# Performance work log

Hardware: AMD Instinct MI355X
Metric: run time of the kernel (lower is better)

The kernel has to match this reference:

```python
import jax, jax.numpy as jnp
import numpy as np
from jax import lax

SEQ, F, H1, H2, B, WV, OBJ, REL, VOCAB = 33, 20480, 900, 900, 2, 100, 35, 82, 117


def setup_inputs() -> dict:
    key = jax.random.key(0)
    ks = jax.random.split(key, 17)
    s = lambda k, shape: jax.random.normal(k, shape, jnp.float32) * 0.02
    return dict(
        x=jax.random.normal(ks[0], (SEQ, B, F), jnp.float32),
        w_ih1=s(ks[1], (4 * H1, F)), w_hh1=s(ks[2], (4 * H1, H1)),
        b_ih1=s(ks[3], (4 * H1,)), b_hh1=s(ks[4], (4 * H1,)),
        w_ih2=s(ks[5], (SEQ, 4 * H2, H1 + WV)), w_hh2=s(ks[6], (SEQ, 4 * H2, H2)),
        b_ih2=s(ks[7], (SEQ, 4 * H2)), b_hh2=s(ks[8], (SEQ, 4 * H2)),
        w_obj1=s(ks[9], (OBJ, H2)), b_obj1=s(ks[10], (OBJ,)),
        w_rel=s(ks[11], (REL, H2)), b_rel=s(ks[12], (REL,)),
        w_obj2=s(ks[13], (OBJ, H2)), b_obj2=s(ks[14], (OBJ,)),
        embed=s(ks[15], (VOCAB, WV)),
    )


def lstm_cell(xt, h, c, w_ih, w_hh, b_ih, b_hh):
    # torch gate order: input, forget, cell(g), output
    gates = xt @ w_ih.T + h @ w_hh.T + b_ih + b_hh
    i, f, g, o = jnp.split(gates, 4, axis=-1)
    c = jax.nn.sigmoid(f) * c + jax.nn.sigmoid(i) * jnp.tanh(g)
    h = jax.nn.sigmoid(o) * jnp.tanh(c)
    return h, c


def reference(x, w_ih1, w_hh1, b_ih1, b_hh1, w_ih2, w_hh2, b_ih2, b_hh2,
              w_obj1, b_obj1, w_rel, b_rel, w_obj2, b_obj2, embed):
    batch = x.shape[1]
    # layer-1 LSTM over full sequence
    def step1(carry, xt):
        h, c = lstm_cell(xt, carry[0], carry[1], w_ih1, w_hh1, b_ih1, b_hh1)
        return (h, c), h
    h0 = jnp.zeros((batch, H1), x.dtype)
    _, out1 = lax.scan(step1, (h0, h0), x)  # [SEQ, B, H1]

    # layer-2: first SEQ-2 cells with zero word vector, distinct weights per step
    wv0 = jnp.zeros((batch, WV), x.dtype)
    def step2(carry, inp):
        xt, wih, whh, bih, bhh = inp
        h, c = lstm_cell(jnp.concatenate([xt, wv0], axis=1), carry[0], carry[1], wih, whh, bih, bhh)
        return (h, c), None
    h20 = jnp.zeros((batch, H2), x.dtype)
    (h2, c2), _ = lax.scan(step2, (h20, h20),
                           (out1[:SEQ - 2], w_ih2[:SEQ - 2], w_hh2[:SEQ - 2],
                            b_ih2[:SEQ - 2], b_hh2[:SEQ - 2]))

    obj1 = h2 @ w_obj1.T + b_obj1                      # [B, 35]
    wv = embed[jnp.argmax(obj1, axis=1)]               # [B, 100]
    h2, c2 = lstm_cell(jnp.concatenate([out1[SEQ - 2], wv], axis=1), h2, c2,
                       w_ih2[SEQ - 2], w_hh2[SEQ - 2], b_ih2[SEQ - 2], b_hh2[SEQ - 2])

    rel = h2 @ w_rel.T + b_rel                         # [B, 82]
    wv = embed[jnp.argmax(rel, axis=1) + OBJ]
    h2, c2 = lstm_cell(jnp.concatenate([out1[SEQ - 1], wv], axis=1), h2, c2,
                       w_ih2[SEQ - 1], w_hh2[SEQ - 1], b_ih2[SEQ - 1], b_hh2[SEQ - 1])

    obj2 = h2 @ w_obj2.T + b_obj2                      # [B, 35]
    return (obj1, rel, obj2)
```

## Files before the change

kernel.cpp:

```cpp
#include <hip/hip_runtime.h>

#define SEQn 33
#define Fn   20480
#define Hn   900
#define Bn   2
#define WVn  100
#define OBJn 35
#define RELn 82
#define G4n  3600
#define Mn   66
#define NBLK 225
#define NITV 37

#define KS1  16
#define KSL1 (Fn/KS1)
#define RB1  15
#define RPB1 240
#define NC1  (KSL1/32)
#define WSTR 40

typedef __attribute__((ext_vector_type(8))) short bf16x8;
typedef __attribute__((ext_vector_type(4))) float f32x4;

__device__ __forceinline__ float sigf(float v){ return 1.f/(1.f+expf(-v)); }
__device__ __forceinline__ float dot4(float4 a, float4 b){ return a.x*b.x+a.y*b.y+a.z*b.z+a.w*b.w; }
__device__ __forceinline__ float wred(float v){
  #pragma unroll
  for (int d = 32; d >= 1; d >>= 1) v += __shfl_xor(v, d, 64);
  return v;
}
__device__ __forceinline__ float gload(const float* p){
  return __hip_atomic_load((const float*)p, __ATOMIC_RELAXED, __HIP_MEMORY_SCOPE_AGENT);
}
__device__ __forceinline__ void gstore(float* p, float v){
  __hip_atomic_store(p, v, __ATOMIC_RELAXED, __HIP_MEMORY_SCOPE_AGENT);
}
__device__ __forceinline__ unsigned short f2bf(float f){
  unsigned u = __float_as_uint(f);
  unsigned r = u + 0x7FFFu + ((u >> 16) & 1u);
  return (unsigned short)(r >> 16);
}
__device__ __forceinline__ float bf2f(unsigned short h){
  return __uint_as_float(((unsigned)h) << 16);
}

__device__ __forceinline__ void gbar(unsigned* bar){
  __syncthreads();
  if (threadIdx.x == 0) {
    unsigned g = __hip_atomic_load(&bar[0], __ATOMIC_RELAXED, __HIP_MEMORY_SCOPE_AGENT);
    unsigned cnt = __hip_atomic_fetch_add(&bar[32], 1u, __ATOMIC_RELAXED, __HIP_MEMORY_SCOPE_AGENT);
    if (cnt == (unsigned)(NBLK-1)) {
      __hip_atomic_store(&bar[32], 0u, __ATOMIC_RELAXED, __HIP_MEMORY_SCOPE_AGENT);
      asm volatile("s_waitcnt vmcnt(0)" ::: "memory");
      __hip_atomic_store(&bar[0], g+1u, __ATOMIC_RELAXED, __HIP_MEMORY_SCOPE_AGENT);
    } else {
      unsigned cur;
      do {
        __builtin_amdgcn_s_sleep(8);
        cur = __hip_atomic_load(&bar[0], __ATOMIC_RELAXED, __HIP_MEMORY_SCOPE_AGENT);
      } while (cur == g);
    }
  }
  __syncthreads();
}

__global__ __launch_bounds__(320) void k1_mfma(
    const float* __restrict__ x, const float* __restrict__ w1,
    float* __restrict__ G1, unsigned* __restrict__ bar)
{
  const int tid = threadIdx.x;
  if (blockIdx.x == 0 && tid == 0) {
    __hip_atomic_store(&bar[0], 0u, __ATOMIC_RELAXED, __HIP_MEMORY_SCOPE_AGENT);
    __hip_atomic_store(&bar[32], 0u, __ATOMIC_RELAXED, __HIP_MEMORY_SCOPE_AGENT);
  }
  __shared__ unsigned short WhL[2][RPB1*WSTR], WlL[2][RPB1*WSTR];
  __shared__ unsigned short XhL[2][80*WSTR],  XlL[2][80*WSTR];

  const int rb = blockIdx.x % RB1;
  const int ks = blockIdx.x / RB1;
  const int r0 = rb * RPB1;
  const int kofs = ks * KSL1;
  const int wv_ = tid >> 6;
  const int lane = tid & 63;
  const int p = lane & 15;
  const int q = lane >> 4;

  f32x4 acc[3][5];
  #pragma unroll
  for (int rt = 0; rt < 3; ++rt)
    #pragma unroll
    for (int mt = 0; mt < 5; ++mt) acc[rt][mt] = (f32x4){0.f,0.f,0.f,0.f};

  float4 wr[6], xrg[2];

  #define ISSUE_STAGE(cc)                                                      \
    { const int kbase = kofs + (cc)*32;                                        \
      _Pragma("unroll")                                                        \
      for (int u = 0; u < 6; ++u) {                                            \
        const int idx = tid + u*320;                                           \
        const int row = idx >> 3, k4 = idx & 7;                                \
        wr[u] = *(const float4*)(w1 + (size_t)(r0+row)*Fn + kbase + k4*4);     \
      }                                                                        \
      _Pragma("unroll")                                                        \
      for (int u = 0; u < 2; ++u) {                                            \
        const int idx = tid + u*320;                                           \
        const int mrow = idx >> 3, k4 = idx & 7;                               \
        xrg[u] = (mrow < Mn)                                                   \
          ? *(const float4*)(x + (size_t)mrow*Fn + kbase + k4*4)               \
          : make_float4(0.f,0.f,0.f,0.f);                                      \
      }                                                                        \
    }

  #define CVTW(dsth, dstl, off, v)                                             \
    { const unsigned short h0=f2bf(v.x), h1=f2bf(v.y), h2=f2bf(v.z), h3=f2bf(v.w); \
      const unsigned short l0=f2bf(v.x-bf2f(h0)), l1=f2bf(v.y-bf2f(h1));       \
      const unsigned short l2=f2bf(v.z-bf2f(h2)), l3=f2bf(v.w-bf2f(h3));       \
      *(uint2*)&dsth[off] = make_uint2((unsigned)h0|((unsigned)h1<<16),        \
                                       (unsigned)h2|((unsigned)h3<<16));       \
      *(uint2*)&dstl[off] = make_uint2((unsigned)l0|((unsigned)l1<<16),        \
                                       (unsigned)l2|((unsigned)l3<<16));       \
    }

  #define WRITE_STAGE(bb)                                                     \
    { _Pragma("unroll")                                                       \
      for (int u = 0; u < 6; ++u) {                                           \
        const int idx = tid + u*320;                                          \
        const int row = idx >> 3, k4 = idx & 7;                               \
        CVTW(WhL[bb], WlL[bb], row*WSTR + k4*4, wr[u]);                       \
      }                                                                       \
      _Pragma("unroll")                                                       \
      for (int u = 0; u < 2; ++u) {                                           \
        const int idx = tid + u*320;                                          \
        const int mrow = idx >> 3, k4 = idx & 7;                              \
        CVTW(XhL[bb], XlL[bb], mrow*WSTR + k4*4, xrg[u]);                     \
      }                                                                       \
    }

  ISSUE_STAGE(0);
  WRITE_STAGE(0);
  __syncthreads();

  for (int c = 0; c < NC1; ++c) {
    const int buf = c & 1;
    if (c+1 < NC1) ISSUE_STAGE(c+1);

    bf16x8 Bh[5], Bl[5];
    #pragma unroll
    for (int mt = 0; mt < 5; ++mt) {
      const int moff = (mt*16 + p)*WSTR + q*8;
      Bh[mt] = *(const bf16x8*)&XhL[buf][moff];
      Bl[mt] = *(const bf16x8*)&XlL[buf][moff];
    }
    #pragma unroll
    for (int rt = 0; rt < 3; ++rt) {
      const int roff = ((wv_ + 5*rt)*16 + p)*WSTR + q*8;
      const bf16x8 Ah = *(const bf16x8*)&WhL[buf][roff];
      const bf16x8 Al = *(const bf16x8*)&WlL[buf][roff];
      #pragma unroll
      for (int mt = 0; mt < 5; ++mt) {
        acc[rt][mt] = __builtin_amdgcn_mfma_f32_16x16x32_bf16(Ah, Bh[mt], acc[rt][mt], 0, 0, 0);
        acc[rt][mt] = __builtin_amdgcn_mfma_f32_16x16x32_bf16(Ah, Bl[mt], acc[rt][mt], 0, 0, 0);
        acc[rt][mt] = __builtin_amdgcn_mfma_f32_16x16x32_bf16(Al, Bh[mt], acc[rt][mt], 0, 0, 0);
      }
    }

    if (c+1 < NC1) WRITE_STAGE(buf^1);
    __syncthreads();
  }

  #pragma unroll
  for (int rt = 0; rt < 3; ++rt)
    #pragma unroll
    for (int mt = 0; mt < 5; ++mt) {
      const int m = mt*16 + p;
      if (m < Mn) {
        #pragma unroll
        for (int r4 = 0; r4 < 4; ++r4) {
          const int grow = r0 + (wv_ + 5*rt)*16 + q*4 + r4;
          atomicAdd(&G1[(size_t)grow*Mn + m], acc[rt][mt][r4]);
        }
      }
    }
  #undef ISSUE_STAGE
  #undef WRITE_STAGE
  #undef CVTW
}

__global__ __launch_bounds__(512) void k_rec(
    const float* __restrict__ G1, float* __restrict__ out1, float* __restrict__ h2buf,
    const float* __restrict__ whh1,
    const float* __restrict__ wih2, const float* __restrict__ whh2,
    const float* __restrict__ bih2, const float* __restrict__ bhh2,
    const float* __restrict__ bih1, const float* __restrict__ bhh1,
    const float* __restrict__ wobj1, const float* __restrict__ bobj1,
    const float* __restrict__ wrel,  const float* __restrict__ brel,
    const float* __restrict__ wobj2, const float* __restrict__ bobj2,
    const float* __restrict__ embed, float* __restrict__ dout,
    unsigned* __restrict__ bar)
{
  __shared__ float hls[Bn][904];
  __shared__ float h2l[Bn][904];
  __shared__ float wvls[Bn][104];
  __shared__ float gls[16][68];
  __shared__ float bls[SEQn][16];
  __shared__ float gexA[16][Bn], gexB[16][Bn];
  __shared__ float cA[4][Bn], cB[4][Bn];
  __shared__ float red[4];
  __shared__ int idxls[Bn];

  const int tid = threadIdx.x;
  const int blk = blockIdx.x;
  const int j0 = blk * 4;
  const int wv_ = tid >> 6;
  const int lane = tid & 63;

  if (tid < 8) {
    const int jj = tid >> 1, m = tid & 1;
    cA[jj][m] = 0.f; cB[jj][m] = 0.f;
    gstore(h2buf + (size_t)m*Hn + j0 + jj, 0.f);
  }

  for (int qq = tid; qq < 16*Mn; qq += 512) {
    const int rho = qq / Mn, t = qq % Mn;
    const int gate = rho >> 2, jj = rho & 3;
    const size_t rA = (size_t)gate*Hn + j0 + jj;
    gls[rho][t] = G1[rA*Mn + t] + bih1[rA] + bhh1[rA];
  }
  for (int qq = tid; qq < SEQn*16; qq += 512) {
    const int s = qq / 16, rho = qq % 16;
    const int gate = rho >> 2, jj = rho & 3;
    const size_t ro = (size_t)s*G4n + (size_t)gate*Hn + j0 + jj;
    bls[s][rho] = bih2[ro] + bhh2[ro];
  }

  float4 wAreg[2][4];
  #pragma unroll
  for (int ri = 0; ri < 2; ++ri) {
    const int rho = wv_*2 + ri;
    const int gate = rho >> 2, jj = rho & 3;
    const size_t row = (size_t)gate*Hn + j0 + jj;
    #pragma unroll
    for (int e = 0; e < 4; ++e) {
      const int k = lane*4 + e*256;
      wAreg[ri][e] = (k <= Hn-4) ? *(const float4*)(whh1 + row*Hn + k)
                                 : make_float4(0.f,0.f,0.f,0.f);
    }
  }

  float4 wiR[2][4], whR[2][4];
  #define ISSUE_W(sp)                                                        \
    { _Pragma("unroll")                                                      \
      for (int ri = 0; ri < 2; ++ri) {                                       \
        const int rho = wv_*2 + ri;                                          \
        const int gate = rho >> 2, jj = rho & 3;                             \
        const size_t ro = (size_t)(sp)*G4n + (size_t)gate*Hn + j0 + jj;      \
        const float* wI = wih2 + ro*1000;                                    \
        const float* wH = whh2 + ro*Hn;                                      \
        _Pragma("unroll")                                                    \
        for (int e = 0; e < 4; ++e) {                                        \
          const int k = lane*4 + e*256;                                      \
          if (k <= 996) wiR[ri][e] = *(const float4*)(wI + k);               \
          if (k <= 896) whR[ri][e] = *(const float4*)(wH + k);               \
        }                                                                    \
      }                                                                      \
    }
  ISSUE_W(0);

  for (int i = 0; i < NITV; ++i) {
    const bool hasA = (i <= 32);
    const int  s = (i >= 1 && i <= 31) ? (i-1) : (i == 33) ? 31 : (i == 35) ? 32 : -1;
    const bool hasB = (s >= 0);

    if (i == 33 || i == 35) {
      if (wv_ < 2) {
        const int m = wv_;
        const int nout = (i == 33) ? OBJn : RELn;
        const int off = (i == 33) ? 0 : Bn*OBJn;
        float v = -1e30f; int idx = 0;
        for (int o = lane; o < nout; o += 64) {
          float t = gload(dout + off + m*nout + o);
          if (t > v) { v = t; idx = o; }
        }
        #pragma unroll
        for (int d = 32; d >= 1; d >>= 1) {
          float ov = __shfl_xor(v, d, 64);
          int   oi = __shfl_xor(idx, d, 64);
          if (ov > v || (ov == v && oi < idx)) { v = ov; idx = oi; }
        }
        if (lane == 0) idxls[m] = idx + ((i == 35) ? OBJn : 0);
      }
      __syncthreads();
      for (int qq = tid; qq < Bn*104; qq += 512) {
        const int m = qq / 104, v4 = qq % 104;
        wvls[m][v4] = (v4 < WVn) ? embed[(size_t)idxls[m]*WVn + v4] : 0.f;
      }
      __syncthreads();
    }

    const bool stageH = hasA || (i == 35);
    const int  srcA = (i == 35) ? 32 : i-1;
    if (stageH) {
      for (int qq = tid; qq < 1808; qq += 512) {
        const int m = qq / 904, kk = qq % 904;
        hls[m][kk] = (i > 0 && kk < 900)
          ? gload(out1 + ((size_t)srcA*Bn + m)*Hn + kk) : 0.f;
      }
    }
    if (hasB) {
      for (int qq = tid; qq < 1808; qq += 512) {
        const int m = qq / 904, kk = qq % 904;
        h2l[m][kk] = (kk < 900)
          ? gload(h2buf + ((size_t)(s&1)*Bn + m)*Hn + kk) : 0.f;
      }
    }
    __syncthreads();

    if (hasA) {
      #pragma unroll
      for (int ri = 0; ri < 2; ++ri) {
        const int rho = wv_*2 + ri;
        float a0 = 0.f, a1 = 0.f;
        #pragma unroll
        for (int e = 0; e < 4; ++e) {
          const int k = lane*4 + e*256;
          if (k <= Hn-4) {
            a0 += dot4(wAreg[ri][e], *(const float4*)&hls[0][k]);
            a1 += dot4(wAreg[ri][e], *(const float4*)&hls[1][k]);
          }
        }
        a0 = wred(a0); a1 = wred(a1);
        if (lane == 0) {
          gexA[rho][0] = a0 + gls[rho][i*Bn + 0];
          gexA[rho][1] = a1 + gls[rho][i*Bn + 1];
        }
      }
    }

    if (hasB) {
      #pragma unroll
      for (int ri = 0; ri < 2; ++ri) {
        const int rho = wv_*2 + ri;
        float b0 = 0.f, b1 = 0.f;
        #pragma unroll
        for (int e = 0; e < 4; ++e) {
          const int k = lane*4 + e*256;
          if (k <= 896) {
            b0 += dot4(wiR[ri][e], *(const float4*)&hls[0][k]);
            b1 += dot4(wiR[ri][e], *(const float4*)&hls[1][k]);
            b0 += dot4(whR[ri][e], *(const float4*)&h2l[0][k]);
            b1 += dot4(whR[ri][e], *(const float4*)&h2l[1][k]);
          } else if (k >= 900 && k <= 996 && s >= SEQn-2) {
            b0 += dot4(wiR[ri][e], *(const float4*)&wvls[0][k-900]);
            b1 += dot4(wiR[ri][e], *(const float4*)&wvls[1][k-900]);
          }
        }
        b0 = wred(b0); b1 = wred(b1);
        if (lane == 0) {
          const float bb = bls[s][rho];
          gexB[rho][0] = b0 + bb;
          gexB[rho][1] = b1 + bb;
        }
      }
      if (s < 32) ISSUE_W(s+1);
    }

    if (i == 32 || i == 34 || i == 36) {
      const int nout = (i == 34) ? RELn : OBJn;
      const float* wh  = (i == 32) ? wobj1 : (i == 34) ? wrel : wobj2;
      const float* bh_ = (i == 32) ? bobj1 : (i == 34) ? brel : bobj2;
      const int off = (i == 32) ? 0 : (i == 34) ? (Bn*OBJn) : (Bn*OBJn + Bn*RELn);
      const int hb = (i == 34) ? 0 : 1;
      if (blk < nout*Bn) {
        const int o = blk >> 1, m = blk & 1;
        float p = 0.f;
        if (tid < 225) {
          const float4 wv4 = *(const float4*)(wh + (size_t)o*Hn + tid*4);
          float* hp = h2buf + ((size_t)hb*Bn + m)*Hn + tid*4;
          p = wv4.x*gload(hp+0) + wv4.y*gload(hp+1)
            + wv4.z*gload(hp+2) + wv4.w*gload(hp+3);
        }
        if (wv_ < 4) {
          const float pr = wred(p);
          if (lane == 0) red[wv_] = pr;
        }
        __syncthreads();
        if (tid == 0)
          gstore(&dout[off + m*nout + o], red[0]+red[1]+red[2]+red[3] + bh_[o]);
      }
    }

    __syncthreads();
    if (tid < 8) {
      const int jj = tid >> 1, m = tid & 1;
      if (hasA) {
        const float cc = sigf(gexA[4+jj][m])*cA[jj][m]
                       + sigf(gexA[jj][m])*tanhf(gexA[8+jj][m]);
        cA[jj][m] = cc;
        gstore(out1 + ((size_t)i*Bn + m)*Hn + j0 + jj, sigf(gexA[12+jj][m])*tanhf(cc));
      }
      if (hasB) {
        const float cc = sigf(gexB[4+jj][m])*cB[jj][m]
                       + sigf(gexB[jj][m])*tanhf(gexB[8+jj][m]);
        cB[jj][m] = cc;
        gstore(h2buf + ((size_t)((s+1)&1)*Bn + m)*Hn + j0 + jj,
               sigf(gexB[12+jj][m])*tanhf(cc));
      }
    }

    if (i < NITV-1) gbar(bar);
  }
  #undef ISSUE_W
}

extern "C" void kernel_launch(void* const* d_in, const int* in_sizes, int n_in,
                              void* d_out, int out_size, void* d_ws, size_t ws_size,
                              hipStream_t stream)
{
  (void)in_sizes; (void)n_in; (void)out_size; (void)ws_size;
  const float* x     = (const float*)d_in[0];
  const float* wih1  = (const float*)d_in[1];
  const float* whh1  = (const float*)d_in[2];
  const float* bih1  = (const float*)d_in[3];
  const float* bhh1  = (const float*)d_in[4];
  const float* wih2  = (const float*)d_in[5];
  const float* whh2  = (const float*)d_in[6];
  const float* bih2  = (const float*)d_in[7];
  const float* bhh2  = (const float*)d_in[8];
  const float* wobj1 = (const float*)d_in[9];
  const float* bobj1 = (const float*)d_in[10];
  const float* wrel  = (const float*)d_in[11];
  const float* brel  = (const float*)d_in[12];
  const float* wobj2 = (const float*)d_in[13];
  const float* bobj2 = (const float*)d_in[14];
  const float* embed = (const float*)d_in[15];
  float* dout = (float*)d_out;

  float* ws = (float*)d_ws;
  float* G1    = ws;
  float* out1  = G1 + (size_t)G4n*Mn;
  float* h2buf = out1 + (size_t)SEQn*Bn*Hn;
  unsigned* bar = (unsigned*)(h2buf + (size_t)2*Bn*Hn);

  hipMemsetAsync(G1, 0, (size_t)G4n*Mn*sizeof(float), stream);
  hipLaunchKernelGGL(k1_mfma, dim3(RB1*KS1), dim3(320), 0, stream, x, wih1, G1, bar);

  void* args[19];
  args[0]  = (void*)&G1;    args[1]  = (void*)&out1;  args[2]  = (void*)&h2buf;
  args[3]  = (void*)&whh1;  args[4]  = (void*)&wih2;  args[5]  = (void*)&whh2;
  args[6]  = (void*)&bih2;  args[7]  = (void*)&bhh2;  args[8]  = (void*)&bih1;
  args[9]  = (void*)&bhh1;  args[10] = (void*)&wobj1; args[11] = (void*)&bobj1;
  args[12] = (void*)&wrel;  args[13] = (void*)&brel;  args[14] = (void*)&wobj2;
  args[15] = (void*)&bobj2; args[16] = (void*)&embed; args[17] = (void*)&dout;
  args[18] = (void*)&bar;
  hipLaunchCooperativeKernel((void*)k_rec, dim3(NBLK), dim3(512), args, 0, stream);
}
```

Measured before the change: 564.6 us.

## Double-buffer layer-2 weight prefetch and peel the steady-state recurrent loop

Splits the persistent recurrent loop into a peeled first step, a fully unrolled steady-state section (iterations 1-31) and a tail section for the argmax and head steps. Layer-2 per-step weights are now double-buffered in two register sets, and the next step's loads are issued before the current step's dot products instead of after them. This gives those loads a whole iteration plus a grid barrier to arrive, and the steady section drops the per-iteration branch logic. The cost is twice the weight registers per thread, which risks spilling or lower occupancy.

```diff
diff --git a/kernel.cpp b/kernel.cpp
--- a/kernel.cpp
+++ b/kernel.cpp
@@ -10,7 +10,6 @@
 #define G4n  3600
 #define Mn   66
 #define NBLK 225
-#define NITV 37
 
 #define KS1  16
 #define KSL1 (Fn/KS1)
@@ -55,9 +54,8 @@
       __hip_atomic_store(&bar[0], g+1u, __ATOMIC_RELAXED, __HIP_MEMORY_SCOPE_AGENT);
     } else {
       unsigned cur;
-      do {
-        __builtin_amdgcn_s_sleep(8);
-        cur = __hip_atomic_load(&bar[0], __ATOMIC_RELAXED, __HIP_MEMORY_SCOPE_AGENT);
+      do { __builtin_amdgcn_s_sleep(8);
+           cur = __hip_atomic_load(&bar[0], __ATOMIC_RELAXED, __HIP_MEMORY_SCOPE_AGENT);
       } while (cur == g);
     }
   }
@@ -247,8 +245,8 @@
     }
   }
 
-  float4 wiR[2][4], whR[2][4];
-  #define ISSUE_W(sp)                                                        \
+  float4 wiR0[2][4], whR0[2][4], wiR1[2][4], whR1[2][4];
+  #define ISSUE_W(sp, WI, WH)                                                \
     { _Pragma("unroll")                                                      \
       for (int ri = 0; ri < 2; ++ri) {                                       \
         const int rho = wv_*2 + ri;                                          \
@@ -259,18 +257,122 @@
         _Pragma("unroll")                                                    \
         for (int e = 0; e < 4; ++e) {                                        \
           const int k = lane*4 + e*256;                                      \
-          if (k <= 996) wiR[ri][e] = *(const float4*)(wI + k);               \
-          if (k <= 896) whR[ri][e] = *(const float4*)(wH + k);               \
+          if (k <= 996) WI[ri][e] = *(const float4*)(wI + k);                \
+          if (k <= 896) WH[ri][e] = *(const float4*)(wH + k);                \
         }                                                                    \
       }                                                                      \
     }
-  ISSUE_W(0);
-
-  for (int i = 0; i < NITV; ++i) {
-    const bool hasA = (i <= 32);
-    const int  s = (i >= 1 && i <= 31) ? (i-1) : (i == 33) ? 31 : (i == 35) ? 32 : -1;
-    const bool hasB = (s >= 0);
-
+
+  #define ADOTS(ivar)                                                        \
+    { _Pragma("unroll")                                                      \
+      for (int ri = 0; ri < 2; ++ri) {                                       \
+        const int rho = wv_*2 + ri;                                          \
+        float a0 = 0.f, a1 = 0.f;                                            \
+        _Pragma("unroll")                                                    \
+        for (int e = 0; e < 4; ++e) {                                        \
+          const int k = lane*4 + e*256;                                      \
+          if (k <= Hn-4) {                                                   \
+            a0 += dot4(wAreg[ri][e], *(const float4*)&hls[0][k]);            \
+            a1 += dot4(wAreg[ri][e], *(const float4*)&hls[1][k]);            \
+          }                                                                  \
+        }                                                                    \
+        a0 = wred(a0); a1 = wred(a1);                                        \
+        if (lane == 0) {                                                     \
+          gexA[rho][0] = a0 + gls[rho][(ivar)*Bn + 0];                       \
+          gexA[rho][1] = a1 + gls[rho][(ivar)*Bn + 1];                       \
+        }                                                                    \
+      }                                                                      \
+    }
+
+  #define BDOTS(svar, WI, WH, USEWV)                                         \
+    { _Pragma("unroll")                                                      \
+      for (int ri = 0; ri < 2; ++ri) {                                       \
+        const int rho = wv_*2 + ri;                                          \
+        float b0 = 0.f, b1 = 0.f;                                            \
+        _Pragma("unroll")                                                    \
+        for (int e = 0; e < 4; ++e) {                                        \
+          const int k = lane*4 + e*256;                                      \
+          if (k <= 896) {                                                    \
+            b0 += dot4(WI[ri][e], *(const float4*)&hls[0][k]);               \
+            b1 += dot4(WI[ri][e], *(const float4*)&hls[1][k]);               \
+            b0 += dot4(WH[ri][e], *(const float4*)&h2l[0][k]);               \
+            b1 += dot4(WH[ri][e], *(const float4*)&h2l[1][k]);               \
+          } else if ((USEWV) && k >= 900 && k <= 996) {                      \
+            b0 += dot4(WI[ri][e], *(const float4*)&wvls[0][k-900]);          \
+            b1 += dot4(WI[ri][e], *(const float4*)&wvls[1][k-900]);          \
+          }                                                                  \
+        }                                                                    \
+        b0 = wred(b0); b1 = wred(b1);                                        \
+        if (lane == 0) {                                                     \
+          const float bb = bls[svar][rho];                                   \
+          gexB[rho][0] = b0 + bb;                                            \
+          gexB[rho][1] = b1 + bb;                                            \
+        }                                                                    \
+      }                                                                      \
+    }
+
+  #define UPD_A(ivar)                                                        \
+    { const float cc = sigf(gexA[4+jj][m])*cA[jj][m]                         \
+                     + sigf(gexA[jj][m])*tanhf(gexA[8+jj][m]);               \
+      cA[jj][m] = cc;                                                        \
+      gstore(out1 + ((size_t)(ivar)*Bn + m)*Hn + j0 + jj,                    \
+             sigf(gexA[12+jj][m])*tanhf(cc)); }
+
+  #define UPD_B(svar)                                                        \
+    { const float cc = sigf(gexB[4+jj][m])*cB[jj][m]                         \
+                     + sigf(gexB[jj][m])*tanhf(gexB[8+jj][m]);               \
+      cB[jj][m] = cc;                                                        \
+      gstore(h2buf + ((size_t)(((svar)+1)&1)*Bn + m)*Hn + j0 + jj,           \
+             sigf(gexB[12+jj][m])*tanhf(cc)); }
+
+  #define STAGE_STEADY(ivar)                                                 \
+    { for (int qq = tid; qq < 1808; qq += 512) {                             \
+        const int m = qq / 904, kk = qq % 904;                               \
+        hls[m][kk] = (kk < 900)                                              \
+          ? gload(out1 + ((size_t)((ivar)-1)*Bn + m)*Hn + kk) : 0.f;         \
+      }                                                                      \
+      for (int qq = tid; qq < 1808; qq += 512) {                             \
+        const int m = qq / 904, kk = qq % 904;                               \
+        h2l[m][kk] = (kk < 900)                                              \
+          ? gload(h2buf + ((size_t)(((ivar)-1)&1)*Bn + m)*Hn + kk) : 0.f;    \
+      } }
+
+  #define STEADY(ivar, WIu, WHu, WIa, WHa)                                   \
+    { STAGE_STEADY(ivar);                                                    \
+      __syncthreads();                                                       \
+      ISSUE_W((ivar), WIa, WHa);                                             \
+      ADOTS(ivar);                                                           \
+      BDOTS((ivar)-1, WIu, WHu, 0);                                          \
+      __syncthreads();                                                       \
+      if (tid < 8) {                                                         \
+        const int jj = tid >> 1, m = tid & 1;                                \
+        UPD_A(ivar);                                                         \
+        UPD_B((ivar)-1);                                                     \
+      }                                                                      \
+      gbar(bar); }
+
+  ISSUE_W(0, wiR0, whR0);
+  __syncthreads();
+
+  if (lane == 0) {
+    #pragma unroll
+    for (int ri = 0; ri < 2; ++ri) {
+      const int rho = wv_*2 + ri;
+      gexA[rho][0] = gls[rho][0];
+      gexA[rho][1] = gls[rho][1];
+    }
+  }
+  __syncthreads();
+  if (tid < 8) { const int jj = tid >> 1, m = tid & 1; UPD_A(0); }
+  gbar(bar);
+
+  for (int ib = 1; ib <= 29; ib += 2) {
+    STEADY(ib,   wiR0, whR0, wiR1, whR1);
+    STEADY(ib+1, wiR1, whR1, wiR0, whR0);
+  }
+  STEADY(31, wiR0, whR0, wiR1, whR1);
+
+  for (int i = 32; i < 37; ++i) {
     if (i == 33 || i == 35) {
       if (wv_ < 2) {
         const int m = wv_;
@@ -297,12 +399,15 @@
       __syncthreads();
     }
 
-    const bool stageH = hasA || (i == 35);
+    const bool hasA = (i == 32);
+    const int  s = (i == 33) ? 31 : (i == 35) ? 32 : -1;
+    const bool hasB = (s >= 0);
     const int  srcA = (i == 35) ? 32 : i-1;
-    if (stageH) {
+
+    if (hasA || i == 35) {
       for (int qq = tid; qq < 1808; qq += 512) {
         const int m = qq / 904, kk = qq % 904;
-        hls[m][kk] = (i > 0 && kk < 900)
+        hls[m][kk] = (kk < 900)
           ? gload(out1 + ((size_t)srcA*Bn + m)*Hn + kk) : 0.f;
       }
     }
@@ -315,54 +420,9 @@
     }
     __syncthreads();
 
-    if (hasA) {
-      #pragma unroll
-      for (int ri = 0; ri < 2; ++ri) {
-        const int rho = wv_*2 + ri;
-        float a0 = 0.f, a1 = 0.f;
-        #pragma unroll
-        for (int e = 0; e < 4; ++e) {
-          const int k = lane*4 + e*256;
-          if (k <= Hn-4) {
-            a0 += dot4(wAreg[ri][e], *(const float4*)&hls[0][k]);
-            a1 += dot4(wAreg[ri][e], *(const float4*)&hls[1][k]);
-          }
-        }
-        a0 = wred(a0); a1 = wred(a1);
-        if (lane == 0) {
-          gexA[rho][0] = a0 + gls[rho][i*Bn + 0];
-          gexA[rho][1] = a1 + gls[rho][i*Bn + 1];
-        }
-      }
-    }
-
-    if (hasB) {
-      #pragma unroll
-      for (int ri = 0; ri < 2; ++ri) {
-        const int rho = wv_*2 + ri;
-        float b0 = 0.f, b1 = 0.f;
-        #pragma unroll
-        for (int e = 0; e < 4; ++e) {
-          const int k = lane*4 + e*256;
-          if (k <= 896) {
-            b0 += dot4(wiR[ri][e], *(const float4*)&hls[0][k]);
-            b1 += dot4(wiR[ri][e], *(const float4*)&hls[1][k]);
-            b0 += dot4(whR[ri][e], *(const float4*)&h2l[0][k]);
-            b1 += dot4(whR[ri][e], *(const float4*)&h2l[1][k]);
-          } else if (k >= 900 && k <= 996 && s >= SEQn-2) {
-            b0 += dot4(wiR[ri][e], *(const float4*)&wvls[0][k-900]);
-            b1 += dot4(wiR[ri][e], *(const float4*)&wvls[1][k-900]);
-          }
-        }
-        b0 = wred(b0); b1 = wred(b1);
-        if (lane == 0) {
-          const float bb = bls[s][rho];
-          gexB[rho][0] = b0 + bb;
-          gexB[rho][1] = b1 + bb;
-        }
-      }
-      if (s < 32) ISSUE_W(s+1);
-    }
+    if (hasA) ADOTS(32);
+    if (i == 33) { BDOTS(31, wiR1, whR1, 1); ISSUE_W(32, wiR0, whR0); }
+    if (i == 35) { BDOTS(32, wiR0, whR0, 1); }
 
     if (i == 32 || i == 34 || i == 36) {
       const int nout = (i == 34) ? RELn : OBJn;
@@ -392,24 +452,20 @@
     __syncthreads();
     if (tid < 8) {
       const int jj = tid >> 1, m = tid & 1;
-      if (hasA) {
-        const float cc = sigf(gexA[4+jj][m])*cA[jj][m]
-                       + sigf(gexA[jj][m])*tanhf(gexA[8+jj][m]);
-        cA[jj][m] = cc;
-        gstore(out1 + ((size_t)i*Bn + m)*Hn + j0 + jj, sigf(gexA[12+jj][m])*tanhf(cc));
-      }
-      if (hasB) {
-        const float cc = sigf(gexB[4+jj][m])*cB[jj][m]
-                       + sigf(gexB[jj][m])*tanhf(gexB[8+jj][m]);
-        cB[jj][m] = cc;
-        gstore(h2buf + ((size_t)((s+1)&1)*Bn + m)*Hn + j0 + jj,
-               sigf(gexB[12+jj][m])*tanhf(cc));
-      }
-    }
-
-    if (i < NITV-1) gbar(bar);
+      if (hasA) UPD_A(32);
+      if (i == 33) UPD_B(31);
+      if (i == 35) UPD_B(32);
+    }
+
+    if (i < 36) gbar(bar);
   }
   #undef ISSUE_W
+  #undef ADOTS
+  #undef BDOTS
+  #undef UPD_A
+  #undef UPD_B
+  #undef STAGE_STEADY
+  #undef STEADY
 }
 
 extern "C" void kernel_launch(void* const* d_in, const int* in_sizes, int n_in,
```

Measured after the change: 675.2 us. +19.6%, slower.

## Specialize recurrent steady-state loop with direct global loads and lighter grid barrier

Applied to the files above, without the earlier changes.

Splits the 37-iteration recurrence into a peeled first step, a specialized loop for steps 1–31 and a tail for the head/argmax steps. The steady-state loop reads h vectors straight from global memory into registers instead of staging them in LDS, and replaces the double-buffered h2 with a per-step history array so reads and writes never alias. It also uses a lighter grid barrier built on raw s_barrier and a shorter sleep in the spin loop. The aim is to cut per-step synchronisation and LDS staging latency on the serial critical path, at the cost of relying on relaxed atomics and waitcnt for memory ordering, which is more fragile.

```diff
diff --git a/kernel.cpp b/kernel.cpp
--- a/kernel.cpp
+++ b/kernel.cpp
@@ -10,7 +10,6 @@
 #define G4n  3600
 #define Mn   66
 #define NBLK 225
-#define NITV 37
 
 #define KS1  16
 #define KSL1 (Fn/KS1)
@@ -55,13 +54,38 @@
       __hip_atomic_store(&bar[0], g+1u, __ATOMIC_RELAXED, __HIP_MEMORY_SCOPE_AGENT);
     } else {
       unsigned cur;
-      do {
-        __builtin_amdgcn_s_sleep(8);
-        cur = __hip_atomic_load(&bar[0], __ATOMIC_RELAXED, __HIP_MEMORY_SCOPE_AGENT);
+      do { __builtin_amdgcn_s_sleep(1);
+           cur = __hip_atomic_load(&bar[0], __ATOMIC_RELAXED, __HIP_MEMORY_SCOPE_AGENT);
       } while (cur == g);
     }
   }
   __syncthreads();
+}
+
+__device__ __forceinline__ void gbar_lite(unsigned* bar, int wv){
+  asm volatile("" ::: "memory");
+  if (wv == 0) asm volatile("s_waitcnt vmcnt(0)" ::: "memory");
+  __builtin_amdgcn_sched_barrier(0);
+  __builtin_amdgcn_s_barrier();
+  __builtin_amdgcn_sched_barrier(0);
+  if (threadIdx.x == 0) {
+    unsigned g = __hip_atomic_load(&bar[0], __ATOMIC_RELAXED, __HIP_MEMORY_SCOPE_AGENT);
+    unsigned cnt = __hip_atomic_fetch_add(&bar[32], 1u, __ATOMIC_RELAXED, __HIP_MEMORY_SCOPE_AGENT);
+    if (cnt == (unsigned)(NBLK-1)) {
+      __hip_atomic_store(&bar[32], 0u, __ATOMIC_RELAXED, __HIP_MEMORY_SCOPE_AGENT);
+      asm volatile("s_waitcnt vmcnt(0)" ::: "memory");
+      __hip_atomic_store(&bar[0], g+1u, __ATOMIC_RELAXED, __HIP_MEMORY_SCOPE_AGENT);
+    } else {
+      unsigned cur;
+      do { __builtin_amdgcn_s_sleep(1);
+           cur = __hip_atomic_load(&bar[0], __ATOMIC_RELAXED, __HIP_MEMORY_SCOPE_AGENT);
+      } while (cur == g);
+    }
+  }
+  __builtin_amdgcn_sched_barrier(0);
+  __builtin_amdgcn_s_barrier();
+  __builtin_amdgcn_sched_barrier(0);
+  asm volatile("" ::: "memory");
 }
 
 __global__ __launch_bounds__(320) void k1_mfma(
@@ -187,7 +211,7 @@
 }
 
 __global__ __launch_bounds__(512) void k_rec(
-    const float* __restrict__ G1, float* __restrict__ out1, float* __restrict__ h2buf,
+    const float* __restrict__ G1, float* __restrict__ out1, float* __restrict__ h2arr,
     const float* __restrict__ whh1,
     const float* __restrict__ wih2, const float* __restrict__ whh2,
     const float* __restrict__ bih2, const float* __restrict__ bhh2,
@@ -217,7 +241,7 @@
   if (tid < 8) {
     const int jj = tid >> 1, m = tid & 1;
     cA[jj][m] = 0.f; cB[jj][m] = 0.f;
-    gstore(h2buf + (size_t)m*Hn + j0 + jj, 0.f);
+    gstore(h2arr + ((size_t)0*Bn + m)*Hn + j0 + jj, 0.f);
   }
 
   for (int qq = tid; qq < 16*Mn; qq += 512) {
@@ -248,7 +272,7 @@
   }
 
   float4 wiR[2][4], whR[2][4];
-  #define ISSUE_W(sp)                                                        \
+  #define ISSUE_W(sp, KMX)                                                   \
     { _Pragma("unroll")                                                      \
       for (int ri = 0; ri < 2; ++ri) {                                       \
         const int rho = wv_*2 + ri;                                          \
@@ -259,18 +283,92 @@
         _Pragma("unroll")                                                    \
         for (int e = 0; e < 4; ++e) {                                        \
           const int k = lane*4 + e*256;                                      \
-          if (k <= 996) wiR[ri][e] = *(const float4*)(wI + k);               \
-          if (k <= 896) whR[ri][e] = *(const float4*)(wH + k);               \
+          if (k <= (KMX)) wiR[ri][e] = *(const float4*)(wI + k);             \
+          if (k <= 896)   whR[ri][e] = *(const float4*)(wH + k);             \
         }                                                                    \
       }                                                                      \
     }
-  ISSUE_W(0);
-
-  for (int i = 0; i < NITV; ++i) {
-    const bool hasA = (i <= 32);
-    const int  s = (i >= 1 && i <= 31) ? (i-1) : (i == 33) ? 31 : (i == 35) ? 32 : -1;
-    const bool hasB = (s >= 0);
-
+
+  #define UPD_A(ivar)                                                        \
+    { const float cc = sigf(gexA[4+jj][m])*cA[jj][m]                         \
+                     + sigf(gexA[jj][m])*tanhf(gexA[8+jj][m]);               \
+      cA[jj][m] = cc;                                                        \
+      gstore(out1 + ((size_t)(ivar)*Bn + m)*Hn + j0 + jj,                    \
+             sigf(gexA[12+jj][m])*tanhf(cc)); }
+
+  #define UPD_B(svar)                                                        \
+    { const float cc = sigf(gexB[4+jj][m])*cB[jj][m]                         \
+                     + sigf(gexB[jj][m])*tanhf(gexB[8+jj][m]);               \
+      cB[jj][m] = cc;                                                        \
+      gstore(h2arr + ((size_t)((svar)+1)*Bn + m)*Hn + j0 + jj,               \
+             sigf(gexB[12+jj][m])*tanhf(cc)); }
+
+  ISSUE_W(0, 896);
+  __syncthreads();
+
+  if (lane == 0) {
+    #pragma unroll
+    for (int ri = 0; ri < 2; ++ri) {
+      const int rho = wv_*2 + ri;
+      gexA[rho][0] = gls[rho][0];
+      gexA[rho][1] = gls[rho][1];
+    }
+  }
+  __syncthreads();
+  if (tid < 8) { const int jj = tid >> 1, m = tid & 1; UPD_A(0); }
+  gbar(bar);
+
+  for (int iv = 1; iv <= 31; ++iv) {
+    const int s = iv - 1;
+    float4 hv[2][4], h2v[2][4];
+    #pragma unroll
+    for (int e = 0; e < 4; ++e) {
+      const int k = lane*4 + e*256;
+      #pragma unroll
+      for (int m = 0; m < 2; ++m) {
+        hv[m][e]  = (k <= 896) ? *(const float4*)(out1  + ((size_t)s*Bn + m)*Hn + k)
+                               : make_float4(0.f,0.f,0.f,0.f);
+        h2v[m][e] = (k <= 896) ? *(const float4*)(h2arr + ((size_t)s*Bn + m)*Hn + k)
+                               : make_float4(0.f,0.f,0.f,0.f);
+      }
+    }
+    #pragma unroll
+    for (int ri = 0; ri < 2; ++ri) {
+      const int rho = wv_*2 + ri;
+      float a0=0.f, a1=0.f, b0=0.f, b1=0.f;
+      #pragma unroll
+      for (int e = 0; e < 4; ++e) {
+        const int k = lane*4 + e*256;
+        if (k <= 896) {
+          a0 += dot4(wAreg[ri][e], hv[0][e]);  a1 += dot4(wAreg[ri][e], hv[1][e]);
+          b0 += dot4(wiR[ri][e],   hv[0][e]);  b1 += dot4(wiR[ri][e],   hv[1][e]);
+          b0 += dot4(whR[ri][e],  h2v[0][e]);  b1 += dot4(whR[ri][e],  h2v[1][e]);
+        }
+      }
+      a0 = wred(a0); a1 = wred(a1); b0 = wred(b0); b1 = wred(b1);
+      if (lane == 0) {
+        gexA[rho][0] = a0 + gls[rho][iv*Bn + 0];
+        gexA[rho][1] = a1 + gls[rho][iv*Bn + 1];
+        const float bb = bls[s][rho];
+        gexB[rho][0] = b0 + bb;
+        gexB[rho][1] = b1 + bb;
+      }
+    }
+    asm volatile("s_waitcnt lgkmcnt(0)" ::: "memory");
+    __builtin_amdgcn_sched_barrier(0);
+    ISSUE_W(iv, (iv >= 31) ? 996 : 896);
+    __builtin_amdgcn_sched_barrier(0);
+    __builtin_amdgcn_s_barrier();
+    __builtin_amdgcn_sched_barrier(0);
+    if (tid < 8) {
+      const int jj = tid >> 1, m = tid & 1;
+      UPD_A(iv);
+      UPD_B(s);
+    }
+    gbar_lite(bar, wv_);
+  }
+
+  for (int i = 32; i < 37; ++i) {
     if (i == 33 || i == 35) {
       if (wv_ < 2) {
         const int m = wv_;
@@ -297,12 +395,15 @@
       __syncthreads();
     }
 
-    const bool stageH = hasA || (i == 35);
+    const bool hasA = (i == 32);
+    const int  s = (i == 33) ? 31 : (i == 35) ? 32 : -1;
+    const bool hasB = (s >= 0);
     const int  srcA = (i == 35) ? 32 : i-1;
-    if (stageH) {
+
+    if (hasA || i == 35) {
       for (int qq = tid; qq < 1808; qq += 512) {
         const int m = qq / 904, kk = qq % 904;
-        hls[m][kk] = (i > 0 && kk < 900)
+        hls[m][kk] = (kk < 900)
           ? gload(out1 + ((size_t)srcA*Bn + m)*Hn + kk) : 0.f;
       }
     }
@@ -310,7 +411,7 @@
       for (int qq = tid; qq < 1808; qq += 512) {
         const int m = qq / 904, kk = qq % 904;
         h2l[m][kk] = (kk < 900)
-          ? gload(h2buf + ((size_t)(s&1)*Bn + m)*Hn + kk) : 0.f;
+          ? gload(h2arr + ((size_t)s*Bn + m)*Hn + kk) : 0.f;
       }
     }
     __syncthreads();
@@ -330,8 +431,8 @@
         }
         a0 = wred(a0); a1 = wred(a1);
         if (lane == 0) {
-          gexA[rho][0] = a0 + gls[rho][i*Bn + 0];
-          gexA[rho][1] = a1 + gls[rho][i*Bn + 1];
+          gexA[rho][0] = a0 + gls[rho][32*Bn + 0];
+          gexA[rho][1] = a1 + gls[rho][32*Bn + 1];
         }
       }
     }
@@ -349,7 +450,7 @@
             b1 += dot4(wiR[ri][e], *(const float4*)&hls[1][k]);
             b0 += dot4(whR[ri][e], *(const float4*)&h2l[0][k]);
             b1 += dot4(whR[ri][e], *(const float4*)&h2l[1][k]);
-          } else if (k >= 900 && k <= 996 && s >= SEQn-2) {
+          } else if (k >= 900 && k <= 996) {
             b0 += dot4(wiR[ri][e], *(const float4*)&wvls[0][k-900]);
             b1 += dot4(wiR[ri][e], *(const float4*)&wvls[1][k-900]);
           }
@@ -361,7 +462,7 @@
           gexB[rho][1] = b1 + bb;
         }
       }
-      if (s < 32) ISSUE_W(s+1);
+      if (i == 33) ISSUE_W(32, 996);
     }
 
     if (i == 32 || i == 34 || i == 36) {
@@ -369,13 +470,13 @@
       const float* wh  = (i == 32) ? wobj1 : (i == 34) ? wrel : wobj2;
       const float* bh_ = (i == 32) ? bobj1 : (i == 34) ? brel : bobj2;
       const int off = (i == 32) ? 0 : (i == 34) ? (Bn*OBJn) : (Bn*OBJn + Bn*RELn);
-      const int hb = (i == 34) ? 0 : 1;
+      const int hb = (i == 32) ? 31 : (i == 34) ? 32 : 33;
       if (blk < nout*Bn) {
         const int o = blk >> 1, m = blk & 1;
         float p = 0.f;
         if (tid < 225) {
           const float4 wv4 = *(const float4*)(wh + (size_t)o*Hn + tid*4);
-          float* hp = h2buf + ((size_t)hb*Bn + m)*Hn + tid*4;
+          const float* hp = h2arr + ((size_t)hb*Bn + m)*Hn + tid*4;
           p = wv4.x*gload(hp+0) + wv4.y*gload(hp+1)
             + wv4.z*gload(hp+2) + wv4.w*gload(hp+3);
         }
@@ -392,24 +493,16 @@
     __syncthreads();
     if (tid < 8) {
       const int jj = tid >> 1, m = tid & 1;
-      if (hasA) {
-        const float cc = sigf(gexA[4+jj][m])*cA[jj][m]
-                       + sigf(gexA[jj][m])*tanhf(gexA[8+jj][m]);
-        cA[jj][m] = cc;
-        gstore(out1 + ((size_t)i*Bn + m)*Hn + j0 + jj, sigf(gexA[12+jj][m])*tanhf(cc));
-      }
-      if (hasB) {
-        const float cc = sigf(gexB[4+jj][m])*cB[jj][m]
-                       + sigf(gexB[jj][m])*tanhf(gexB[8+jj][m]);
-        cB[jj][m] = cc;
-        gstore(h2buf + ((size_t)((s+1)&1)*Bn + m)*Hn + j0 + jj,
-               sigf(gexB[12+jj][m])*tanhf(cc));
-      }
-    }
-
-    if (i < NITV-1) gbar(bar);
+      if (hasA) UPD_A(32);
+      if (i == 33) UPD_B(31);
+      if (i == 35) UPD_B(32);
+    }
+
+    if (i < 36) gbar(bar);
   }
   #undef ISSUE_W
+  #undef UPD_A
+  #undef UPD_B
 }
 
 extern "C" void kernel_launch(void* const* d_in, const int* in_sizes, int n_in,
@@ -438,14 +531,14 @@
   float* ws = (float*)d_ws;
   float* G1    = ws;
   float* out1  = G1 + (size_t)G4n*Mn;
-  float* h2buf = out1 + (size_t)SEQn*Bn*Hn;
-  unsigned* bar = (unsigned*)(h2buf + (size_t)2*Bn*Hn);
+  float* h2arr = out1 + (size_t)SEQn*Bn*Hn;
+  unsigned* bar = (unsigned*)(h2arr + (size_t)34*Bn*Hn);
 
   hipMemsetAsync(G1, 0, (size_t)G4n*Mn*sizeof(float), stream);
   hipLaunchKernelGGL(k1_mfma, dim3(RB1*KS1), dim3(320), 0, stream, x, wih1, G1, bar);
 
   void* args[19];
-  args[0]  = (void*)&G1;    args[1]  = (void*)&out1;  args[2]  = (void*)&h2buf;
+  args[0]  = (void*)&G1;    args[1]  = (void*)&out1;  args[2]  = (void*)&h2arr;
   args[3]  = (void*)&whh1;  args[4]  = (void*)&wih2;  args[5]  = (void*)&whh2;
   args[6]  = (void*)&bih2;  args[7]  = (void*)&bhh2;  args[8]  = (void*)&bih1;
   args[9]  = (void*)&bhh1;  args[10] = (void*)&wobj1; args[11] = (void*)&bobj1;
```

Result: faster. 500.2 us (-11.4%).
